# Optimization experiments

Hardware: AMD Instinct MI355X
Metric: run time of the kernel (lower is better)

## Reference

```python
import jax, jax.numpy as jnp
import numpy as np

NUM_EMBEDDING = 8192
EMBEDDING_DIM = 512
BS = 16384
NEG_SLOPE = 0.01  # torch LeakyReLU default


def setup_inputs() -> dict:
    key = jax.random.key(0)
    k1, k2, k3, k4, k5, k6, k7 = jax.random.split(key, 7)
    d, K = EMBEDDING_DIM, NUM_EMBEDDING
    s1 = 1.0 / np.sqrt(d)
    return {
        "encoded_eeg": jax.random.normal(k1, (BS, d), dtype=jnp.float32),
        "encoded_mel": jax.random.normal(k2, (BS, d), dtype=jnp.float32),
        "embeddings": jax.random.normal(k3, (K, d), dtype=jnp.float32),
        "W1": jax.random.uniform(k4, (d, d), jnp.float32, -s1, s1),
        "b1": jax.random.uniform(k5, (d,), jnp.float32, -s1, s1),
        "W2": jax.random.uniform(k6, (K, d), jnp.float32, -s1, s1),
        "b2": jax.random.uniform(k7, (K,), jnp.float32, -s1, s1),
    }


def reference(encoded_eeg, encoded_mel, embeddings, W1, b1, W2, b2):
    # --- nearest-codebook indices for mel (detached in original) ---
    flat_mel = encoded_mel.reshape(-1, EMBEDDING_DIM)
    dists = (jnp.sum(embeddings ** 2, axis=1)[None, :]
             + jnp.sum(flat_mel ** 2, axis=1, keepdims=True)
             - 2.0 * flat_mel @ embeddings.T)  # [BS, K]
    mel_indices = jnp.argmin(dists, axis=-1)  # [BS]

    # --- small MLP logits over eeg ---
    flat_eeg = encoded_eeg.reshape(-1, EMBEDDING_DIM)
    h = flat_eeg @ W1.T + b1
    h = jnp.where(h >= 0, h, NEG_SLOPE * h)  # LeakyReLU
    logits = h @ W2.T + b2  # [BS, K]

    eeg_indices = jnp.argmax(logits, axis=-1)
    acc_rate = jnp.mean((eeg_indices == mel_indices).astype(jnp.float32))

    # cross entropy (mean over batch)
    logp = jax.nn.log_softmax(logits, axis=-1)
    loss = -jnp.mean(jnp.take_along_axis(logp, mel_indices[:, None], axis=1))
    return (loss, acc_rate)
```

## Files before the change

kernel.cpp:

```cpp
#include <hip/hip_runtime.h>
#include <hip/hip_bf16.h>
#include <hip/hip_fp8.h>

#define BSZ 16384
#define DIM 512
#define NEMB 8192
#define NEG 0.01f
#define NSPLIT 8
#define NG 128

typedef __attribute__((ext_vector_type(8))) short short8;
typedef __attribute__((ext_vector_type(4))) float f32x4;
typedef __attribute__((ext_vector_type(2))) long long2v;
typedef __attribute__((ext_vector_type(4))) int i32x4;
typedef __attribute__((ext_vector_type(8))) int i32x8;

typedef const __attribute__((address_space(1))) void GVT;
typedef __attribute__((address_space(3))) void LVT;

__device__ __forceinline__ void gl_lds16(const void* g, void* l) {
    __builtin_amdgcn_global_load_lds((GVT*)g, (LVT*)l, 16, 0, 0);
}

__device__ __forceinline__ float bf2f(unsigned short u) {
    union { unsigned int i; float f; } c; c.i = ((unsigned int)u) << 16; return c.f;
}
__device__ __forceinline__ unsigned short f2bf(float f) {
    union { __hip_bfloat16 h; unsigned short u; } c; c.h = __float2bfloat16(f); return c.u;
}
__device__ __forceinline__ unsigned char f2fp8(float f) {
    __hip_fp8_e4m3 t(f); return (unsigned char)t.__x;
}
__device__ __forceinline__ unsigned int fkey(float f) {
    unsigned int u = __float_as_uint(f);
    return u ^ ((unsigned int)((int)u >> 31) | 0x80000000u);
}

__device__ __forceinline__ size_t pack_addr(int r, int k) {
    int kg = k >> 6, ko = k & 63;
    int half = ko >> 5, lq = (ko & 31) >> 3, sub = ko & 7;
    int L = lq * 16 + (r & 15);
    return ((size_t)((r >> 4) * 8 + kg) << 10) + (size_t)(L << 4) + (half << 3) + sub;
}

__device__ __forceinline__ void pipe_barrier2() {
    asm volatile("s_waitcnt vmcnt(2) lgkmcnt(0)\ns_barrier" ::: "memory");
}
__device__ __forceinline__ void plain_barrier() {
    asm volatile("s_barrier" ::: "memory");
}
__device__ __forceinline__ void drain_vm() {
    asm volatile("s_waitcnt vmcnt(0)" ::: "memory");
}

#define ISSUE_B(G, BUF) do { \
    int Gm = (G) & (NG - 1); \
    size_t boff = ((size_t)(Gm >> 3) << 15) + (size_t)((Gm & 7) << 10); \
    gl_lds16(gB8 + boff, &sB8[BUF][uWd]); \
} while (0)

#define COMPUTE8(KP, SA, SB) do { \
    i32x8 fb[4]; \
    _Pragma("unroll") for (int i = 0; i < 4; i++) { \
        i32x4 bl = *(const i32x4*)&sB8[SA][offB[i]]; \
        i32x4 bh = *(const i32x4*)&sB8[SB][offB[i]]; \
        fb[i] = __builtin_shufflevector(bl, bh, 0, 1, 2, 3, 4, 5, 6, 7); \
    } \
    __builtin_amdgcn_s_setprio(1); \
    _Pragma("unroll") for (int mi = 0; mi < 2; mi++) \
        _Pragma("unroll") for (int ni = 0; ni < 4; ni++) \
            acc[mi][ni] = __builtin_amdgcn_mfma_scale_f32_16x16x128_f8f6f4( \
                fa8[mi][KP], fb[ni], acc[mi][ni], 0, 0, 0, 0x7F7F7F7Fu, 0, 0x7F7F7F7Fu); \
    __builtin_amdgcn_s_setprio(0); \
} while (0)

#define EPILOGUE(NT) do { \
    int c0off = (NT) << 6; \
    if (is_logits) { \
        _Pragma("unroll") for (int ni = 0; ni < 4; ni++) { \
            int j = c0off + ni * 16 + l15; \
            float bb = sAux[j]; \
            unsigned int ic = (unsigned int)(NEMB - 1 - (nbase + j)); \
            _Pragma("unroll") for (int mi = 0; mi < 2; mi++) \
                _Pragma("unroll") for (int rg = 0; rg < 4; rg++) { \
                    float logit = acc[mi][ni][rg] + bb; \
                    int r = mi * 4 + rg; \
                    s[r] += __expf(logit); \
                    unsigned int pk = (fkey(logit) & 0xFFFFE000u) | ic; \
                    pbest[r] = pbest[r] > pk ? pbest[r] : pk; \
                    acc[mi][ni][rg] = 0.f; \
                } \
        } \
    } else { \
        _Pragma("unroll") for (int ni = 0; ni < 4; ni++) { \
            int j = c0off + ni * 16 + l15; \
            float en = sAux[j]; \
            unsigned int cl = (unsigned int)(nbase + j); \
            _Pragma("unroll") for (int mi = 0; mi < 2; mi++) \
                _Pragma("unroll") for (int rg = 0; rg < 4; rg++) { \
                    float d = fmaf(-2.f, acc[mi][ni][rg], en); \
                    unsigned int pk = (fkey(d) & 0xFFFFE000u) | cl; \
                    int r = mi * 4 + rg; \
                    pbest[r] = pbest[r] < pk ? pbest[r] : pk; \
                    acc[mi][ni][rg] = 0.f; \
                } \
        } \
    } \
} while (0)

__global__ void k_prep(const float* __restrict__ eeg, const float* __restrict__ mel,
                       const float* __restrict__ emb, const float* __restrict__ W2,
                       const float* __restrict__ W1,
                       unsigned short* __restrict__ o_eeg, unsigned short* __restrict__ o_w1,
                       unsigned char* __restrict__ o_mel8, unsigned char* __restrict__ o_emb8,
                       unsigned char* __restrict__ o_w28,
                       float* __restrict__ enorm,
                       float* __restrict__ acc2, int* __restrict__ cnt) {
    int bid = blockIdx.x, tid = threadIdx.x;
    if (bid == 0 && tid == 0) { acc2[0] = 0.f; acc2[1] = 0.f; *cnt = 0; }
    if (bid < 1024) {
        const int n_big = BSZ * DIM / 4;
        const int n_mid = NEMB * DIM / 4;
        const int n_w1  = DIM * DIM / 4;
        const int total = n_big * 2 + n_mid * 2 + n_w1;
        for (int i = bid * 256 + tid; i < total; i += 1024 * 256) {
            int j = i;
            if (j < n_big) {
                float4 v = ((const float4*)eeg)[j];
                ushort4 o; o.x = f2bf(v.x); o.y = f2bf(v.y); o.z = f2bf(v.z); o.w = f2bf(v.w);
                ((ushort4*)o_eeg)[j] = o;
            } else if ((j -= n_big) < n_w1) {
                float4 v = ((const float4*)W1)[j];
                ushort4 o; o.x = f2bf(v.x); o.y = f2bf(v.y); o.z = f2bf(v.z); o.w = f2bf(v.w);
                ((ushort4*)o_w1)[j] = o;
            } else if ((j -= n_w1) < n_big) {
                float4 v = ((const float4*)mel)[j];
                uchar4 o; o.x = f2fp8(v.x); o.y = f2fp8(v.y); o.z = f2fp8(v.z); o.w = f2fp8(v.w);
                *(uchar4*)(o_mel8 + pack_addr(j >> 7, (j & 127) * 4)) = o;
            } else if ((j -= n_big) < n_mid) {
                float4 v = ((const float4*)emb)[j];
                uchar4 o; o.x = f2fp8(v.x); o.y = f2fp8(v.y); o.z = f2fp8(v.z); o.w = f2fp8(v.w);
                *(uchar4*)(o_emb8 + pack_addr(j >> 7, (j & 127) * 4)) = o;
            } else {
                j -= n_mid;
                float4 v = ((const float4*)W2)[j];
                uchar4 o; o.x = f2fp8(v.x); o.y = f2fp8(v.y); o.z = f2fp8(v.z); o.w = f2fp8(v.w);
                *(uchar4*)(o_w28 + pack_addr(j >> 7, (j & 127) * 4)) = o;
            }
        }
    } else {
        int w = tid >> 6, lane = tid & 63;
        int row0 = (bid - 1024) * 8 + w * 2;
        #pragma unroll
        for (int t = 0; t < 2; t++) {
            int row = row0 + t;
            const float4* p = (const float4*)(emb + (size_t)row * DIM) + lane * 2;
            float4 a = p[0], b = p[1];
            float s = a.x*a.x + a.y*a.y + a.z*a.z + a.w*a.w
                    + b.x*b.x + b.y*b.y + b.z*b.z + b.w*b.w;
            #pragma unroll
            for (int d = 1; d < 64; d <<= 1) s += __shfl_xor(s, d);
            if (lane == 0) enorm[row] = s;
        }
    }
}

__launch_bounds__(256, 2)
__global__ void k_hgemm(const unsigned short* __restrict__ A,
                        const unsigned short* __restrict__ B,
                        const float* __restrict__ b1,
                        unsigned short* __restrict__ H,
                        unsigned char* __restrict__ H8) {
    __shared__ __align__(16) unsigned short sA[4096], sB[4096];
    int tid = threadIdx.x;
    int w = tid >> 6, lane = tid & 63;
    int wr = w >> 1, wc = w & 1;
    int lquad = lane >> 4, l15 = lane & 15;
    int mt = blockIdx.x >> 2, nt = blockIdx.x & 3;
    int m0 = mt * 128, n0 = nt * 128;

    int e0 = w * 512 + lane * 8;
    int r0 = e0 >> 5, ce = e0 & 31;
    const unsigned short* gA0 = A + (m0 + r0) * DIM + ce;
    const unsigned short* gA1 = gA0 + 64 * DIM;
    const unsigned short* gB0 = B + (n0 + r0) * DIM + ce;
    const unsigned short* gB1 = gB0 + 64 * DIM;
    unsigned short* lA0 = sA + w * 512;  unsigned short* lA1 = sA + (w + 4) * 512;
    unsigned short* lB0 = sB + w * 512;  unsigned short* lB1 = sB + (w + 4) * 512;

    int offA[4], offB[4];
    #pragma unroll
    for (int i = 0; i < 4; i++) {
        offA[i] = (wr * 64 + i * 16 + l15) * 32 + lquad * 8;
        offB[i] = (wc * 64 + i * 16 + l15) * 32 + lquad * 8;
    }

    f32x4 acc[4][4];
    #pragma unroll
    for (int mi = 0; mi < 4; mi++)
        #pragma unroll
        for (int ni = 0; ni < 4; ni++) acc[mi][ni] = 0;

    for (int kk = 0; kk < 16; kk++) {
        gl_lds16(gA0, lA0); gl_lds16(gA1, lA1);
        gl_lds16(gB0, lB0); gl_lds16(gB1, lB1);
        gA0 += 32; gA1 += 32; gB0 += 32; gB1 += 32;
        __syncthreads();
        short8 af[4], bf_[4];
        #pragma unroll
        for (int i = 0; i < 4; i++) {
            af[i]  = *(const short8*)&sA[offA[i]];
            bf_[i] = *(const short8*)&sB[offB[i]];
        }
        #pragma unroll
        for (int mi = 0; mi < 4; mi++)
            #pragma unroll
            for (int ni = 0; ni < 4; ni++)
                acc[mi][ni] = __builtin_amdgcn_mfma_f32_16x16x32_bf16(af[mi], bf_[ni], acc[mi][ni], 0, 0, 0);
        __syncthreads();
    }

    #pragma unroll
    for (int ni = 0; ni < 4; ni++) {
        int col = n0 + wc * 64 + ni * 16 + l15;
        float bv = b1[col];
        #pragma unroll
        for (int mi = 0; mi < 4; mi++) {
            int rowb = m0 + wr * 64 + mi * 16 + lquad * 4;
            #pragma unroll
            for (int rg = 0; rg < 4; rg++) {
                float v = acc[mi][ni][rg] + bv;
                v = v >= 0.f ? v : NEG * v;
                H[(rowb + rg) * DIM + col] = f2bf(v);
                H8[pack_addr(rowb + rg, col)] = f2fp8(v);
            }
        }
    }
}

__launch_bounds__(256, 3)
__global__ void k_big(const unsigned char* __restrict__ Mel8,
                      const unsigned char* __restrict__ Emb8,
                      const unsigned char* __restrict__ H8,
                      const unsigned char* __restrict__ W28,
                      const float* __restrict__ enorm,
                      const float* __restrict__ b2,
                      float* __restrict__ p_s,
                      unsigned int* __restrict__ p_pmax,
                      unsigned int* __restrict__ p_pmin) {
    __shared__ __align__(16) unsigned char sB8[4][4096];
    __shared__ float sAux[1024];
    int tid = threadIdx.x;
    int w = tid >> 6, lane = tid & 63;
    int lquad = lane >> 4, l15 = lane & 15;
    int bid = blockIdx.x;
    int is_logits = bid & 1;
    int id = bid >> 1;
    int mt = id >> 3, split = id & 7;
    int m0 = mt * 128, nbase = split * (NEMB / NSPLIT);

    int uWd = w * 1024;
    const unsigned char* gAb = (is_logits ? H8 : Mel8);
    const unsigned char* gB8 = (is_logits ? W28 : Emb8) + (size_t)(nbase + 16 * w) * 512 + lane * 16;

    int offB[4];
    #pragma unroll
    for (int i = 0; i < 4; i++) offB[i] = i * 1024 + lane * 16;

    #pragma unroll
    for (int j = 0; j < 4; j++) {
        int c = tid + j * 256;
        sAux[c] = is_logits ? b2[nbase + c] : (enorm[nbase + c] - 512.0f);
    }

    i32x8 fa8[2][4];
    #pragma unroll
    for (int mi = 0; mi < 2; mi++)
        #pragma unroll
        for (int kp = 0; kp < 4; kp++) {
            const unsigned char* p = gAb
                + ((size_t)(((m0 >> 4) + 2 * w + mi) * 8 + 2 * kp) << 10) + lane * 16;
            i32x4 lo = *(const i32x4*)p;
            i32x4 hi = *(const i32x4*)(p + 1024);
            fa8[mi][kp] = __builtin_shufflevector(lo, hi, 0, 1, 2, 3, 4, 5, 6, 7);
        }
    drain_vm();

    ISSUE_B(0, 0);
    ISSUE_B(1, 1);
    ISSUE_B(2, 2);
    ISSUE_B(3, 3);

    f32x4 acc[2][4];
    #pragma unroll
    for (int mi = 0; mi < 2; mi++)
        #pragma unroll
        for (int ni = 0; ni < 4; ni++) acc[mi][ni] = 0;

    float s[8];
    unsigned int pbest[8];
    unsigned int pinit = is_logits ? 0u : 0xFFFFFFFFu;
    #pragma unroll
    for (int r = 0; r < 8; r++) { s[r] = 0.f; pbest[r] = pinit; }

    for (int gg = 0; gg < NG; gg += 8) {
        pipe_barrier2(); COMPUTE8(0, 0, 1); plain_barrier(); ISSUE_B(gg + 4, 0); ISSUE_B(gg + 5, 1);
        pipe_barrier2(); COMPUTE8(1, 2, 3); plain_barrier(); ISSUE_B(gg + 6, 2); ISSUE_B(gg + 7, 3);
        pipe_barrier2(); COMPUTE8(2, 0, 1); plain_barrier(); ISSUE_B(gg + 8, 0); ISSUE_B(gg + 9, 1);
        pipe_barrier2(); COMPUTE8(3, 2, 3); plain_barrier(); ISSUE_B(gg + 10, 2); ISSUE_B(gg + 11, 3);
        EPILOGUE(gg >> 3);
    }

    if (is_logits) {
        #pragma unroll
        for (int r = 0; r < 8; r++)
            #pragma unroll
            for (int d = 1; d < 16; d <<= 1) {
                s[r] += __shfl_xor(s[r], d);
                unsigned int o = (unsigned int)__shfl_xor((int)pbest[r], d);
                pbest[r] = pbest[r] > o ? pbest[r] : o;
            }
        if (l15 == 0) {
            #pragma unroll
            for (int mi = 0; mi < 2; mi++)
                #pragma unroll
                for (int rg = 0; rg < 4; rg++) {
                    int row = w * 32 + mi * 16 + lquad * 4 + rg;
                    int pidx = split * BSZ + m0 + row;
                    p_s[pidx] = s[mi * 4 + rg];
                    p_pmax[pidx] = pbest[mi * 4 + rg];
                }
        }
    } else {
        #pragma unroll
        for (int r = 0; r < 8; r++)
            #pragma unroll
            for (int d = 1; d < 16; d <<= 1) {
                unsigned int o = (unsigned int)__shfl_xor((int)pbest[r], d);
                pbest[r] = pbest[r] < o ? pbest[r] : o;
            }
        if (l15 == 0) {
            #pragma unroll
            for (int mi = 0; mi < 2; mi++)
                #pragma unroll
                for (int rg = 0; rg < 4; rg++) {
                    int row = w * 32 + mi * 16 + lquad * 4 + rg;
                    p_pmin[split * BSZ + m0 + row] = pbest[mi * 4 + rg];
                }
        }
    }
}

__global__ void k_tail(const float* __restrict__ p_s, const unsigned int* __restrict__ p_pmax,
                       const unsigned int* __restrict__ p_pmin,
                       const unsigned short* __restrict__ H,
                       const float* __restrict__ W2,
                       const float* __restrict__ b2,
                       float* __restrict__ acc2, int* __restrict__ cnt,
                       float* __restrict__ out) {
    __shared__ int s_idx[256];
    __shared__ float s_l1[256], s_match[256];
    __shared__ float s_d[4];
    int bid = blockIdx.x, tid = threadIdx.x;
    int w = tid >> 6, lane = tid & 63;
    int r = bid * 256 + tid;

    float S = 0.f; unsigned int PM = 0u, PN = 0xFFFFFFFFu;
    #pragma unroll
    for (int sp = 0; sp < NSPLIT; sp++) {
        S += p_s[sp * BSZ + r];
        unsigned int a = p_pmax[sp * BSZ + r];
        PM = PM > a ? PM : a;
        unsigned int b = p_pmin[sp * BSZ + r];
        PN = PN < b ? PN : b;
    }
    int eidx = (NEMB - 1) - (int)(PM & 0x1FFFu);
    int midx = (int)(PN & 0x1FFFu);
    s_idx[tid] = midx;
    s_l1[tid] = __logf(S) - b2[midx];
    s_match[tid] = (eidx == midx) ? 1.f : 0.f;
    __syncthreads();

    float d0 = 0.f, d1 = 0.f;
    for (int j = 0; j < 64; j++) {
        int rr = w * 64 + j;
        int ridx = s_idx[rr];
        uint4 hv = *(const uint4*)(H + (size_t)(bid * 256 + rr) * DIM + lane * 8);
        const float4* wp = (const float4*)(W2 + (size_t)ridx * DIM + lane * 8);
        float4 w0 = wp[0], w1 = wp[1];
        float p = bf2f((unsigned short)(hv.x & 0xffff)) * w0.x + bf2f((unsigned short)(hv.x >> 16)) * w0.y
                + bf2f((unsigned short)(hv.y & 0xffff)) * w0.z + bf2f((unsigned short)(hv.y >> 16)) * w0.w
                + bf2f((unsigned short)(hv.z & 0xffff)) * w1.x + bf2f((unsigned short)(hv.z >> 16)) * w1.y
                + bf2f((unsigned short)(hv.w & 0xffff)) * w1.z + bf2f((unsigned short)(hv.w >> 16)) * w1.w;
        if (j & 1) d1 += p; else d0 += p;
    }
    float ds = d0 + d1;
    #pragma unroll
    for (int d = 1; d < 64; d <<= 1) ds += __shfl_xor(ds, d);
    if (lane == 0) s_d[w] = ds;

    __syncthreads();
    for (int st = 128; st > 0; st >>= 1) {
        if (tid < st) { s_l1[tid] += s_l1[tid + st]; s_match[tid] += s_match[tid + st]; }
        __syncthreads();
    }
    if (tid == 0) {
        float loss_blk = s_l1[0] - (s_d[0] + s_d[1] + s_d[2] + s_d[3]);
        atomicAdd(&acc2[0], loss_blk * (1.0f / BSZ));
        atomicAdd(&acc2[1], s_match[0] * (1.0f / BSZ));
        __threadfence();
        if (atomicAdd(cnt, 1) == 63) {
            float L = atomicAdd(&acc2[0], 0.f);
            float M = atomicAdd(&acc2[1], 0.f);
            out[0] = L; out[1] = M;
        }
    }
}

extern "C" void kernel_launch(void* const* d_in, const int* in_sizes, int n_in,
                              void* d_out, int out_size, void* d_ws, size_t ws_size,
                              hipStream_t stream) {
    const float* eeg = (const float*)d_in[0];
    const float* mel = (const float*)d_in[1];
    const float* emb = (const float*)d_in[2];
    const float* W1  = (const float*)d_in[3];
    const float* b1  = (const float*)d_in[4];
    const float* W2  = (const float*)d_in[5];
    const float* b2  = (const float*)d_in[6];
    float* out = (float*)d_out;

    unsigned short* ws_eeg = (unsigned short*)d_ws;
    unsigned short* ws_w1  = ws_eeg + (size_t)BSZ * DIM;
    unsigned short* ws_h   = ws_w1  + (size_t)DIM * DIM;
    unsigned char*  ws_h8  = (unsigned char*)(ws_h + (size_t)BSZ * DIM);
    unsigned char*  ws_mel8 = ws_h8  + (size_t)BSZ * DIM;
    unsigned char*  ws_emb8 = ws_mel8 + (size_t)BSZ * DIM;
    unsigned char*  ws_w28  = ws_emb8 + (size_t)NEMB * DIM;
    float* ws_en  = (float*)(ws_w28 + (size_t)NEMB * DIM);
    float* p_s    = ws_en + NEMB;
    unsigned int* p_pmax = (unsigned int*)(p_s + (size_t)NSPLIT * BSZ);
    unsigned int* p_pmin = p_pmax + (size_t)NSPLIT * BSZ;
    float* acc2   = (float*)(p_pmin + (size_t)NSPLIT * BSZ);
    int*   cnt    = (int*)(acc2 + 2);

    k_prep<<<2048, 256, 0, stream>>>(eeg, mel, emb, W2, W1,
                                     ws_eeg, ws_w1, ws_mel8, ws_emb8, ws_w28,
                                     ws_en, acc2, cnt);
    k_hgemm<<<(BSZ / 128) * (DIM / 128), 256, 0, stream>>>(ws_eeg, ws_w1, b1, ws_h, ws_h8);
    k_big<<<(BSZ / 128) * NSPLIT * 2, 256, 0, stream>>>(ws_mel8, ws_emb8, ws_h8, ws_w28,
                                                        ws_en, b2, p_s, p_pmax, p_pmin);
    k_tail<<<BSZ / 256, 256, 0, stream>>>(p_s, p_pmax, p_pmin, ws_h, W2, b2, acc2, cnt, out);
}
```

Before: 352.9 us.

## Load B fragments directly from global memory instead of LDS pipeline

Removes the LDS staging buffers, the global_load_lds prefetch pipeline and the per-step barriers. Each wave now reads its B-operand MFMA fragments straight from global memory in the packed layout. Block index mapping is also reordered so the 8 splits of one M tile are adjacent, which should improve L2 reuse of A. This cuts barrier and LDS traffic, but each of the four waves now fetches the full B tile itself (4x redundant global/L2 reads) with no explicit prefetch, so load latency may be exposed.

```diff
diff --git a/kernel.cpp b/kernel.cpp
--- a/kernel.cpp
+++ b/kernel.cpp
@@ -7,11 +7,9 @@
 #define NEMB 8192
 #define NEG 0.01f
 #define NSPLIT 8
-#define NG 128
 
 typedef __attribute__((ext_vector_type(8))) short short8;
 typedef __attribute__((ext_vector_type(4))) float f32x4;
-typedef __attribute__((ext_vector_type(2))) long long2v;
 typedef __attribute__((ext_vector_type(4))) int i32x4;
 typedef __attribute__((ext_vector_type(8))) int i32x8;
 
@@ -42,37 +40,6 @@
     int L = lq * 16 + (r & 15);
     return ((size_t)((r >> 4) * 8 + kg) << 10) + (size_t)(L << 4) + (half << 3) + sub;
 }
-
-__device__ __forceinline__ void pipe_barrier2() {
-    asm volatile("s_waitcnt vmcnt(2) lgkmcnt(0)\ns_barrier" ::: "memory");
-}
-__device__ __forceinline__ void plain_barrier() {
-    asm volatile("s_barrier" ::: "memory");
-}
-__device__ __forceinline__ void drain_vm() {
-    asm volatile("s_waitcnt vmcnt(0)" ::: "memory");
-}
-
-#define ISSUE_B(G, BUF) do { \
-    int Gm = (G) & (NG - 1); \
-    size_t boff = ((size_t)(Gm >> 3) << 15) + (size_t)((Gm & 7) << 10); \
-    gl_lds16(gB8 + boff, &sB8[BUF][uWd]); \
-} while (0)
-
-#define COMPUTE8(KP, SA, SB) do { \
-    i32x8 fb[4]; \
-    _Pragma("unroll") for (int i = 0; i < 4; i++) { \
-        i32x4 bl = *(const i32x4*)&sB8[SA][offB[i]]; \
-        i32x4 bh = *(const i32x4*)&sB8[SB][offB[i]]; \
-        fb[i] = __builtin_shufflevector(bl, bh, 0, 1, 2, 3, 4, 5, 6, 7); \
-    } \
-    __builtin_amdgcn_s_setprio(1); \
-    _Pragma("unroll") for (int mi = 0; mi < 2; mi++) \
-        _Pragma("unroll") for (int ni = 0; ni < 4; ni++) \
-            acc[mi][ni] = __builtin_amdgcn_mfma_scale_f32_16x16x128_f8f6f4( \
-                fa8[mi][KP], fb[ni], acc[mi][ni], 0, 0, 0, 0x7F7F7F7Fu, 0, 0x7F7F7F7Fu); \
-    __builtin_amdgcn_s_setprio(0); \
-} while (0)
 
 #define EPILOGUE(NT) do { \
     int c0off = (NT) << 6; \
@@ -248,24 +215,18 @@
                       float* __restrict__ p_s,
                       unsigned int* __restrict__ p_pmax,
                       unsigned int* __restrict__ p_pmin) {
-    __shared__ __align__(16) unsigned char sB8[4][4096];
     __shared__ float sAux[1024];
     int tid = threadIdx.x;
     int w = tid >> 6, lane = tid & 63;
     int lquad = lane >> 4, l15 = lane & 15;
     int bid = blockIdx.x;
-    int is_logits = bid & 1;
-    int id = bid >> 1;
-    int mt = id >> 3, split = id & 7;
+    int split = bid & 7;
+    int is_logits = (bid >> 3) & 1;
+    int mt = bid >> 4;
     int m0 = mt * 128, nbase = split * (NEMB / NSPLIT);
 
-    int uWd = w * 1024;
     const unsigned char* gAb = (is_logits ? H8 : Mel8);
-    const unsigned char* gB8 = (is_logits ? W28 : Emb8) + (size_t)(nbase + 16 * w) * 512 + lane * 16;
-
-    int offB[4];
-    #pragma unroll
-    for (int i = 0; i < 4; i++) offB[i] = i * 1024 + lane * 16;
+    const unsigned char* gBb = (is_logits ? W28 : Emb8);
 
     #pragma unroll
     for (int j = 0; j < 4; j++) {
@@ -284,12 +245,9 @@
             i32x4 hi = *(const i32x4*)(p + 1024);
             fa8[mi][kp] = __builtin_shufflevector(lo, hi, 0, 1, 2, 3, 4, 5, 6, 7);
         }
-    drain_vm();
-
-    ISSUE_B(0, 0);
-    ISSUE_B(1, 1);
-    ISSUE_B(2, 2);
-    ISSUE_B(3, 3);
+    __syncthreads();
+
+    const unsigned char* gB0 = gBb + (((size_t)(nbase >> 4) * 8) << 10) + lane * 16;
 
     f32x4 acc[2][4];
     #pragma unroll
@@ -303,12 +261,28 @@
     #pragma unroll
     for (int r = 0; r < 8; r++) { s[r] = 0.f; pbest[r] = pinit; }
 
-    for (int gg = 0; gg < NG; gg += 8) {
-        pipe_barrier2(); COMPUTE8(0, 0, 1); plain_barrier(); ISSUE_B(gg + 4, 0); ISSUE_B(gg + 5, 1);
-        pipe_barrier2(); COMPUTE8(1, 2, 3); plain_barrier(); ISSUE_B(gg + 6, 2); ISSUE_B(gg + 7, 3);
-        pipe_barrier2(); COMPUTE8(2, 0, 1); plain_barrier(); ISSUE_B(gg + 8, 0); ISSUE_B(gg + 9, 1);
-        pipe_barrier2(); COMPUTE8(3, 2, 3); plain_barrier(); ISSUE_B(gg + 10, 2); ISSUE_B(gg + 11, 3);
-        EPILOGUE(gg >> 3);
+    for (int nt = 0; nt < 16; nt++) {
+        const unsigned char* pB = gB0 + (size_t)nt * 32768;
+        #pragma unroll
+        for (int kp = 0; kp < 4; kp++) {
+            i32x8 fb[4];
+            #pragma unroll
+            for (int ni = 0; ni < 4; ni++) {
+                const unsigned char* q = pB + ni * 8192 + kp * 2048;
+                i32x4 lo = *(const i32x4*)q;
+                i32x4 hi = *(const i32x4*)(q + 1024);
+                fb[ni] = __builtin_shufflevector(lo, hi, 0, 1, 2, 3, 4, 5, 6, 7);
+            }
+            __builtin_amdgcn_s_setprio(1);
+            #pragma unroll
+            for (int mi = 0; mi < 2; mi++)
+                #pragma unroll
+                for (int ni = 0; ni < 4; ni++)
+                    acc[mi][ni] = __builtin_amdgcn_mfma_scale_f32_16x16x128_f8f6f4(
+                        fa8[mi][kp], fb[ni], acc[mi][ni], 0, 0, 0, 0x7F7F7F7Fu, 0, 0x7F7F7F7Fu);
+            __builtin_amdgcn_s_setprio(0);
+        }
+        EPILOGUE(nt);
     }
 
     if (is_logits) {
```

After: 360.4 us. +2.1%, slower.
